# Kernel tuning notes

Measured on AMD Instinct MI355X. Metric: run time of the kernel, lower is better.

Reference implementation:

```python
import jax, jax.numpy as jnp
import numpy as np
import math

D_MODEL = 1024
N_HEADS = 16
D_HEAD = D_MODEL // N_HEADS  # 64
ROPE_BASE = 10000.0


def make_inv_freq(dim: int, base: float = ROPE_BASE) -> jnp.ndarray:
    half = dim // 2
    if half == 0:
        return jnp.zeros((1,), dtype=jnp.float32)
    return jnp.asarray(1.0 / base ** (np.arange(half, dtype=np.float32) * 2.0 / dim))


def rope_1d(x, pos, inv_freq):
    # x: (B, H, L, d_slice); pos: (B, 1, L)
    D = x.shape[-1]
    half = D // 2
    if half == 0:
        return x
    f = pos[..., None].astype(jnp.float32) * inv_freq  # (B,1,L,half)
    c, s = jnp.cos(f), jnp.sin(f)
    x1, x2 = x[..., :half], x[..., half:2 * half]
    out = jnp.concatenate([x1 * c - x2 * s, x2 * c + x1 * s], axis=-1)
    if D > 2 * half:
        out = jnp.concatenate([out, x[..., 2 * half:]], axis=-1)
    return out


def rope_3d(x, rows, cols, pairs):
    # x: (B, H, L, D_HEAD); rows/cols/pairs: (B, L)
    d_per = D_HEAD // 3
    d_row = D_HEAD - 2 * d_per  # 22
    d_col = d_per               # 21
    d1, d2 = d_row, d_row + d_col
    r = rows[:, None, :]
    c = cols[:, None, :]
    p = pairs[:, None, :]
    x_row = rope_1d(x[..., :d1], r, make_inv_freq(d_row))
    x_col = rope_1d(x[..., d1:d2], c, make_inv_freq(d_col))
    x_pair = rope_1d(x[..., d2:], p, make_inv_freq(d_per))
    return jnp.concatenate([x_row, x_col, x_pair], axis=-1)


def setup_inputs() -> dict:
    key = jax.random.key(0)
    ks = jax.random.split(key, 8)
    B, L, D = 2, 2048, D_MODEL
    x = jax.random.normal(ks[0], (B, L, D), dtype=jnp.float32)
    rows = jax.random.randint(ks[1], (B, L), 0, 30, dtype=jnp.int32)
    cols = jax.random.randint(ks[2], (B, L), 0, 30, dtype=jnp.int32)
    pairs = jax.random.randint(ks[3], (B, L), 0, 8, dtype=jnp.int32)
    key_padding_mask = jnp.ones((B, L), dtype=bool)
    scale = 0.02
    Wq = jax.random.normal(ks[4], (D, D), dtype=jnp.float32) * scale
    Wk = jax.random.normal(ks[5], (D, D), dtype=jnp.float32) * scale
    Wv = jax.random.normal(ks[6], (D, D), dtype=jnp.float32) * scale
    Wo = jax.random.normal(ks[7], (D, D), dtype=jnp.float32) * scale
    return {"x": x, "rows": rows, "cols": cols, "pairs": pairs,
            "key_padding_mask": key_padding_mask,
            "Wq": Wq, "Wk": Wk, "Wv": Wv, "Wo": Wo}


def reference(x, rows, cols, pairs, key_padding_mask, Wq, Wk, Wv, Wo):
    B, L, D = x.shape
    H, Dh = N_HEADS, D_HEAD
    # torch Linear (bias=False): y = x @ W.T, W: (out, in)
    q = jnp.einsum('bld,ed->ble', x, Wq).reshape(B, L, H, Dh).transpose(0, 2, 1, 3)
    k = jnp.einsum('bld,ed->ble', x, Wk).reshape(B, L, H, Dh).transpose(0, 2, 1, 3)
    v = jnp.einsum('bld,ed->ble', x, Wv).reshape(B, L, H, Dh).transpose(0, 2, 1, 3)
    # 3-axis RoPE per head (self-attention: same positions for q and k)
    q = rope_3d(q, rows, cols, pairs)
    k = rope_3d(k, rows, cols, pairs)
    scale = math.sqrt(Dh)
    scores = jnp.einsum('bhqd,bhkd->bhqk', q, k) / scale
    scores = jnp.where(key_padding_mask[:, None, None, :], scores, -jnp.inf)
    attn = jax.nn.softmax(scores, axis=-1)
    out = jnp.einsum('bhqk,bhkd->bhqd', attn, v)
    out = out.transpose(0, 2, 1, 3).reshape(B, L, D)
    return jnp.einsum('bld,ed->ble', out, Wo)
```

## Files before the change

kernel.cpp:

```cpp
#include <hip/hip_runtime.h>

typedef unsigned short ushort_t;
typedef __bf16 bf16x8 __attribute__((ext_vector_type(8)));
typedef float f32x4 __attribute__((ext_vector_type(4)));

#define LOG10K 9.210340371976184f
#define QSCALE 0.18033688011112042f

__device__ __forceinline__ unsigned short f2b(float f) {
  unsigned u = __float_as_uint(f);
  u += 0x7fffu + ((u >> 16) & 1u);
  return (unsigned short)(u >> 16);
}
__device__ __forceinline__ float b2f(unsigned short h) {
  return __uint_as_float(((unsigned)h) << 16);
}
__device__ __forceinline__ float exp2_fast(float x) {
  float r;
  asm("v_exp_f32 %0, %1" : "=v"(r) : "v"(x));
  return r;
}

__device__ __forceinline__ void async16(const void* g, void* l) {
  __builtin_amdgcn_global_load_lds(
      (const __attribute__((address_space(1))) unsigned int*)g,
      (__attribute__((address_space(3))) unsigned int*)l, 16, 0, 0);
}

__global__ void cvt_f32_bf16(const float* __restrict__ src, ushort_t* __restrict__ dst, int n4) {
  int i = blockIdx.x * blockDim.x + threadIdx.x;
  int stride = gridDim.x * blockDim.x;
  for (; i < n4; i += stride) {
    float4 v = ((const float4*)src)[i];
    ushort4 o;
    o.x = f2b(v.x); o.y = f2b(v.y); o.z = f2b(v.z); o.w = f2b(v.w);
    ((ushort4*)dst)[i] = o;
  }
}

__global__ void cvt_w4(const float* __restrict__ a, const float* __restrict__ b,
                       const float* __restrict__ c, const float* __restrict__ d,
                       ushort_t* __restrict__ dst) {
  int blk = blockIdx.x;
  int w = blk >> 10;
  int i = (blk & 1023) * 256 + threadIdx.x;
  const float* src = (w == 0) ? a : (w == 1) ? b : (w == 2) ? c : d;
  float4 v = ((const float4*)src)[i];
  ushort4 o;
  o.x = f2b(v.x); o.y = f2b(v.y); o.z = f2b(v.z); o.w = f2b(v.w);
  ((ushort4*)dst)[(size_t)w * 262144 + i] = o;
}

template<int OUTMODE>
__global__ __launch_bounds__(256) void gemm_bt(const ushort_t* __restrict__ A,
                                               const ushort_t* __restrict__ Bw,
                                               void* __restrict__ out,
                                               void* __restrict__ out2,
                                               void* __restrict__ out3,
                                               int M, int N, int K) {
  __shared__ ushort_t As[128 * 64];
  __shared__ ushort_t Bs[128 * 64];
  int tid = threadIdx.x;
  int w = tid >> 6, l = tid & 63, g = l >> 4, c = l & 15;
  int nbx = gridDim.x;
  int lin = blockIdx.y * nbx + blockIdx.x;
  int per = (nbx * gridDim.y) >> 3;
  int swz = (lin & 7) * per + (lin >> 3);
  int m0 = (swz / nbx) * 128, n0 = (swz % nbx) * 128;
  int wm = (w >> 1) * 64, wn = (w & 1) * 64;
  f32x4 acc[4][4] = {};

  for (int kt = 0; kt < K; kt += 64) {
#pragma unroll
    for (int cc = 0; cc < 4; ++cc) {
      int e = cc * 2048 + w * 512 + l * 8;
      int row = e >> 6;
      int jb = l & 7;
      int col = (jb ^ (row & 7)) << 3;
      async16(A + (size_t)(m0 + row) * K + kt + col, As + row * 64 + jb * 8);
      async16(Bw + (size_t)(n0 + row) * K + kt + col, Bs + row * 64 + jb * 8);
    }
    __syncthreads();
#pragma unroll
    for (int s = 0; s < 2; ++s) {
      bf16x8 af[4], bfr[4];
#pragma unroll
      for (int mi = 0; mi < 4; ++mi) {
        int row = wm + mi * 16 + c;
        int blk = (s * 4 + g) ^ (row & 7);
        af[mi] = *(const bf16x8*)(const void*)(As + row * 64 + blk * 8);
      }
#pragma unroll
      for (int ni = 0; ni < 4; ++ni) {
        int row = wn + ni * 16 + c;
        int blk = (s * 4 + g) ^ (row & 7);
        bfr[ni] = *(const bf16x8*)(const void*)(Bs + row * 64 + blk * 8);
      }
#pragma unroll
      for (int mi = 0; mi < 4; ++mi)
#pragma unroll
        for (int ni = 0; ni < 4; ++ni)
          acc[mi][ni] = __builtin_amdgcn_mfma_f32_16x16x32_bf16(af[mi], bfr[ni], acc[mi][ni], 0, 0, 0);
    }
    __syncthreads();
  }

#pragma unroll
  for (int mi = 0; mi < 4; ++mi) {
#pragma unroll
    for (int ni = 0; ni < 4; ++ni) {
      int mrow0 = m0 + wm + mi * 16 + g * 4;
      int ncol = n0 + wn + ni * 16 + c;
      if (OUTMODE == 3) {
        int sec = ncol >> 10;
        int nn = ncol & 1023;
        int h = nn >> 6, d = nn & 63;
        int b = mrow0 >> 11, ll0 = mrow0 & 2047;
        if (sec == 2) {
          ushort4 o;
          o.x = f2b(acc[mi][ni][0]); o.y = f2b(acc[mi][ni][1]);
          o.z = f2b(acc[mi][ni][2]); o.w = f2b(acc[mi][ni][3]);
          *(ushort4*)((ushort_t*)out3 + ((size_t)(b * 16 + h) * 64 + d) * 2048 + ll0) = o;
        } else {
          ushort_t* dst = (ushort_t*)(sec ? out2 : out);
#pragma unroll
          for (int j = 0; j < 4; ++j)
            dst[((size_t)(b * 16 + h) * 2048 + ll0 + j) * 64 + d] = f2b(acc[mi][ni][j]);
        }
      } else {
#pragma unroll
        for (int j = 0; j < 4; ++j)
          ((float*)out)[(size_t)(mrow0 + j) * N + ncol] = acc[mi][ni][j];
      }
    }
  }
}

__global__ void rope_qk(ushort_t* __restrict__ Qg, ushort_t* __restrict__ Kg,
                        const int* __restrict__ rows, const int* __restrict__ cols,
                        const int* __restrict__ pairs) {
  __shared__ float tl[1420];
  for (int i = threadIdx.x; i < 710; i += 256) {
    float ang;
    if (i < 330) {
      int p = i / 11, k = i - p * 11;
      ang = (float)p * __expf(-(LOG10K / 11.0f) * (float)k);
    } else if (i < 630) {
      int r = i - 330;
      int p = r / 10, k = r - p * 10;
      ang = (float)p * __expf(-(LOG10K * 2.0f / 21.0f) * (float)k);
    } else {
      int r = i - 630;
      int p = r / 10, k = r - p * 10;
      ang = (float)p * __expf(-(LOG10K * 2.0f / 21.0f) * (float)k);
    }
    float s, cs;
    sincosf(ang, &s, &cs);
    tl[2 * i] = cs;
    tl[2 * i + 1] = s;
  }
  __syncthreads();
  const float2* rt = (const float2*)tl;
  const float2* ct = (const float2*)(tl + 660);
  const float2* pt = (const float2*)(tl + 1260);

  int idx = blockIdx.x * blockDim.x + threadIdx.x;
  int which = idx >> 16;
  int r = idx & 65535;
  int b = r >> 15;
  int h = (r >> 11) & 15;
  int ll = r & 2047;
  ushort_t* base = (which ? Kg : Qg) + ((size_t)(b * 16 + h) * 2048 + ll) * 64;

  float f[64];
  const uint4* p = (const uint4*)base;
#pragma unroll
  for (int t = 0; t < 8; ++t) {
    uint4 v = p[t];
    unsigned a0 = v.x, a1 = v.y, a2 = v.z, a3 = v.w;
    f[t * 8 + 0] = b2f((unsigned short)(a0 & 0xffff)); f[t * 8 + 1] = b2f((unsigned short)(a0 >> 16));
    f[t * 8 + 2] = b2f((unsigned short)(a1 & 0xffff)); f[t * 8 + 3] = b2f((unsigned short)(a1 >> 16));
    f[t * 8 + 4] = b2f((unsigned short)(a2 & 0xffff)); f[t * 8 + 5] = b2f((unsigned short)(a2 >> 16));
    f[t * 8 + 6] = b2f((unsigned short)(a3 & 0xffff)); f[t * 8 + 7] = b2f((unsigned short)(a3 >> 16));
  }

  int bl = b * 2048 + ll;
  int pr = rows[bl], pc = cols[bl], pp = pairs[bl];

#pragma unroll
  for (int i = 0; i < 11; ++i) {
    float2 cs = rt[pr * 11 + i];
    float x1 = f[i], x2 = f[i + 11];
    f[i] = x1 * cs.x - x2 * cs.y;
    f[i + 11] = x2 * cs.x + x1 * cs.y;
  }
#pragma unroll
  for (int i = 0; i < 10; ++i) {
    float2 cs = ct[pc * 10 + i];
    float x1 = f[22 + i], x2 = f[32 + i];
    f[22 + i] = x1 * cs.x - x2 * cs.y;
    f[32 + i] = x2 * cs.x + x1 * cs.y;
    float2 cs2 = pt[pp * 10 + i];
    x1 = f[43 + i]; x2 = f[53 + i];
    f[43 + i] = x1 * cs2.x - x2 * cs2.y;
    f[53 + i] = x2 * cs2.x + x1 * cs2.y;
  }
  if (which == 0) {
#pragma unroll
    for (int i = 0; i < 64; ++i) f[i] *= QSCALE;
  }

  uint4* po = (uint4*)base;
#pragma unroll
  for (int t = 0; t < 8; ++t) {
    uint4 v;
    v.x = (unsigned)f2b(f[t * 8 + 0]) | ((unsigned)f2b(f[t * 8 + 1]) << 16);
    v.y = (unsigned)f2b(f[t * 8 + 2]) | ((unsigned)f2b(f[t * 8 + 3]) << 16);
    v.z = (unsigned)f2b(f[t * 8 + 4]) | ((unsigned)f2b(f[t * 8 + 5]) << 16);
    v.w = (unsigned)f2b(f[t * 8 + 6]) | ((unsigned)f2b(f[t * 8 + 7]) << 16);
    po[t] = v;
  }
}

__global__ __launch_bounds__(512) void flash_attn(const ushort_t* __restrict__ Qg,
                                                  const ushort_t* __restrict__ Kg,
                                                  const ushort_t* __restrict__ Vt,
                                                  ushort_t* __restrict__ AO) {
  __shared__ ushort_t Kl[2][4096];
  __shared__ ushort_t Vl[2][4096];
  __shared__ ushort_t Pl[8][1024];
  int bid = blockIdx.x;
  int wg = (bid & 7) * 64 + (bid >> 3);
  int bh = wg >> 4, qt = wg & 15;
  int tid = threadIdx.x;
  int w = tid >> 6, l = tid & 63, g = l >> 4, c = l & 15;

  const ushort_t* Qbase = Qg + ((size_t)bh * 2048 + qt * 128 + w * 16) * 64;
  bf16x8 qf[2];
#pragma unroll
  for (int s = 0; s < 2; ++s)
    qf[s] = *(const bf16x8*)(const void*)(Qbase + c * 64 + s * 32 + g * 8);

  f32x4 acc[4] = {};
  float mrow = -1e30f;
  float lrow = 0.f;

  char* KlB = (char*)&Kl[0][0];
  char* VlB = (char*)&Vl[0][0];
  char* PlW = (char*)&Pl[w][0];
  int c7 = c & 7;
  int c7_4 = c7 << 4;
  int offA0 = c * 128 + ((g ^ c7) << 4);
  int offA1 = c * 128 + (((4 ^ g) ^ c7) << 4);
  char* prow = PlW + c * 128;

  int srow = tid >> 3, sjb = tid & 7;
  int scol = (sjb ^ (srow & 7)) << 3;
  char* Kdst = KlB + srow * 128 + sjb * 16;
  char* Vdst = VlB + srow * 128 + sjb * 16;
  const ushort_t* Ksrc = Kg + ((size_t)bh * 2048 + srow) * 64 + scol;
  const ushort_t* Vsrc = Vt + ((size_t)bh * 64 + srow) * 2048 + scol;

  async16(Ksrc, Kdst);
  async16(Vsrc, Vdst);
  Ksrc += 4096; Vsrc += 64;
  asm volatile("s_waitcnt vmcnt(0)" ::: "memory");
  __syncthreads();

  int bufoff = 0;
  for (int kt = 0; kt < 32; ++kt) {
    if (kt < 31) {
      async16(Ksrc, Kdst + (bufoff ^ 8192));
      async16(Vsrc, Vdst + (bufoff ^ 8192));
      Ksrc += 4096; Vsrc += 64;
    }
    const char* KA0 = KlB + bufoff + offA0;
    const char* KA1 = KlB + bufoff + offA1;
    const char* VA0 = VlB + bufoff + offA0;
    const char* VA1 = VlB + bufoff + offA1;

    f32x4 sc[4] = {};
    __builtin_amdgcn_s_setprio(1);
#pragma unroll
    for (int kb = 0; kb < 4; ++kb) {
      bf16x8 a0 = *(const bf16x8*)(const void*)(KA0 + kb * 2048);
      bf16x8 a1 = *(const bf16x8*)(const void*)(KA1 + kb * 2048);
      sc[kb] = __builtin_amdgcn_mfma_f32_16x16x32_bf16(a0, qf[0], sc[kb], 0, 0, 0);
      sc[kb] = __builtin_amdgcn_mfma_f32_16x16x32_bf16(a1, qf[1], sc[kb], 0, 0, 0);
    }
    __builtin_amdgcn_s_setprio(0);

    {
      float t = sc[0][0];
#pragma unroll
      for (int kb = 0; kb < 4; ++kb)
#pragma unroll
        for (int j = 0; j < 4; ++j) t = fmaxf(t, sc[kb][j]);
      t = fmaxf(t, __shfl_xor(t, 16));
      t = fmaxf(t, __shfl_xor(t, 32));
      if (!__all(t - mrow <= 8.0f)) {
        float mnew = fmaxf(mrow, t);
        float corr = exp2_fast(mrow - mnew);
        mrow = mnew;
        lrow *= corr;
#pragma unroll
        for (int j = 0; j < 4; ++j) {
          float cj = __shfl(corr, ((l >> 4) << 2) | j);
#pragma unroll
          for (int db = 0; db < 4; ++db) acc[db][j] *= cj;
        }
      }
      float m = mrow;
      float ps = 0.f;
#pragma unroll
      for (int kb = 0; kb < 4; ++kb) {
        float p0 = exp2_fast(sc[kb][0] - m);
        float p1 = exp2_fast(sc[kb][1] - m);
        float p2 = exp2_fast(sc[kb][2] - m);
        float p3 = exp2_fast(sc[kb][3] - m);
        ps += (p0 + p1) + (p2 + p3);
        unsigned r0, r1;
        asm("v_cvt_pk_bf16_f32 %0, %1, %2" : "=v"(r0) : "v"(p0), "v"(p1));
        asm("v_cvt_pk_bf16_f32 %0, %1, %2" : "=v"(r1) : "v"(p2), "v"(p3));
        uint2 pr; pr.x = r0; pr.y = r1;
        *(uint2*)(prow + ((kb * 32 + g * 8) ^ c7_4)) = pr;
      }
      ps += __shfl_xor(ps, 16);
      ps += __shfl_xor(ps, 32);
      lrow += ps;
    }
    asm volatile("s_waitcnt lgkmcnt(0)" ::: "memory");

    __builtin_amdgcn_s_setprio(1);
#pragma unroll
    for (int s2 = 0; s2 < 2; ++s2) {
      bf16x8 pf = *(const bf16x8*)(const void*)(prow + ((s2 * 64 + g * 16) ^ c7_4));
      const char* VA = s2 ? VA1 : VA0;
#pragma unroll
      for (int db = 0; db < 4; ++db) {
        bf16x8 vf = *(const bf16x8*)(const void*)(VA + db * 2048);
        acc[db] = __builtin_amdgcn_mfma_f32_16x16x32_bf16(pf, vf, acc[db], 0, 0, 0);
      }
    }
    __builtin_amdgcn_s_setprio(0);

    asm volatile("s_waitcnt vmcnt(0)" ::: "memory");
    __syncthreads();
    bufoff ^= 8192;
  }

  int b = bh >> 4, h = bh & 15;
  {
    float linv = 1.0f / lrow;
#pragma unroll
    for (int j = 0; j < 4; ++j) {
      float inv = __shfl(linv, ((l >> 4) << 2) | j);
      int token = qt * 128 + w * 16 + g * 4 + j;
      size_t rowbase = (size_t)(b * 2048 + token) * 1024 + h * 64;
#pragma unroll
      for (int db = 0; db < 4; ++db)
        AO[rowbase + db * 16 + c] = f2b(acc[db][j] * inv);
    }
  }
}

extern "C" void kernel_launch(void* const* d_in, const int* in_sizes, int n_in,
                              void* d_out, int out_size, void* d_ws, size_t ws_size,
                              hipStream_t stream) {
  const float* x = (const float*)d_in[0];
  const int* rows = (const int*)d_in[1];
  const int* cols = (const int*)d_in[2];
  const int* pairs = (const int*)d_in[3];
  const float* Wq = (const float*)d_in[5];
  const float* Wk = (const float*)d_in[6];
  const float* Wv = (const float*)d_in[7];
  const float* Wo = (const float*)d_in[8];

  char* ws = (char*)d_ws;
  ushort_t* xb   = (ushort_t*)(ws);
  ushort_t* Wqkv = (ushort_t*)(ws + (8u << 20));
  ushort_t* Wob  = Wqkv + 3u * 1048576u;
  ushort_t* Qg   = (ushort_t*)(ws + (16u << 20));
  ushort_t* Kg   = (ushort_t*)(ws + (24u << 20));
  ushort_t* Vt   = (ushort_t*)(ws + (32u << 20));
  ushort_t* AO   = (ushort_t*)(ws);

  cvt_f32_bf16<<<1024, 256, 0, stream>>>(x, xb, 4194304 / 4);
  cvt_w4<<<4096, 256, 0, stream>>>(Wq, Wk, Wv, Wo, Wqkv);

  dim3 gg3(24, 32);
  gemm_bt<3><<<gg3, 256, 0, stream>>>(xb, Wqkv, Qg, Kg, Vt, 4096, 3072, 1024);

  rope_qk<<<512, 256, 0, stream>>>(Qg, Kg, rows, cols, pairs);

  flash_attn<<<512, 512, 0, stream>>>(Qg, Kg, Vt, AO);

  dim3 gg2(8, 32);
  gemm_bt<2><<<gg2, 256, 0, stream>>>(AO, Wob, d_out, nullptr, nullptr, 4096, 1024, 1024);
}
```

Before: 131.1 us.

## Triple-buffer K/V tiles, defer row-sum reduction, and fuse conversion kernels

New measurement: 125.4 us. 1.05x faster.

```diff
diff --git a/kernel.cpp b/kernel.cpp
--- a/kernel.cpp
+++ b/kernel.cpp
@@ -27,28 +27,29 @@
       (__attribute__((address_space(3))) unsigned int*)l, 16, 0, 0);
 }
 
-__global__ void cvt_f32_bf16(const float* __restrict__ src, ushort_t* __restrict__ dst, int n4) {
-  int i = blockIdx.x * blockDim.x + threadIdx.x;
-  int stride = gridDim.x * blockDim.x;
-  for (; i < n4; i += stride) {
-    float4 v = ((const float4*)src)[i];
+__global__ void cvt_all(const float* __restrict__ x, const float* __restrict__ a,
+                        const float* __restrict__ b, const float* __restrict__ cw,
+                        const float* __restrict__ d,
+                        ushort_t* __restrict__ xb, ushort_t* __restrict__ wb) {
+  int i = blockIdx.x * 256 + threadIdx.x;
+#pragma unroll
+  for (int it = 0; it < 2; ++it) {
+    int idx = i + it * 524288;
+    float4 v = ((const float4*)x)[idx];
     ushort4 o;
     o.x = f2b(v.x); o.y = f2b(v.y); o.z = f2b(v.z); o.w = f2b(v.w);
-    ((ushort4*)dst)[i] = o;
-  }
-}
-
-__global__ void cvt_w4(const float* __restrict__ a, const float* __restrict__ b,
-                       const float* __restrict__ c, const float* __restrict__ d,
-                       ushort_t* __restrict__ dst) {
-  int blk = blockIdx.x;
-  int w = blk >> 10;
-  int i = (blk & 1023) * 256 + threadIdx.x;
-  const float* src = (w == 0) ? a : (w == 1) ? b : (w == 2) ? c : d;
-  float4 v = ((const float4*)src)[i];
-  ushort4 o;
-  o.x = f2b(v.x); o.y = f2b(v.y); o.z = f2b(v.z); o.w = f2b(v.w);
-  ((ushort4*)dst)[(size_t)w * 262144 + i] = o;
+    ((ushort4*)xb)[idx] = o;
+  }
+#pragma unroll
+  for (int it = 0; it < 2; ++it) {
+    int idx = i + it * 524288;
+    int w = idx >> 18, off = idx & 262143;
+    const float* src = (w == 0) ? a : (w == 1) ? b : (w == 2) ? cw : d;
+    float4 v = ((const float4*)src)[off];
+    ushort4 o;
+    o.x = f2b(v.x); o.y = f2b(v.y); o.z = f2b(v.z); o.w = f2b(v.w);
+    ((ushort4*)wb)[idx] = o;
+  }
 }
 
 template<int OUTMODE>
@@ -226,8 +227,8 @@
                                                   const ushort_t* __restrict__ Kg,
                                                   const ushort_t* __restrict__ Vt,
                                                   ushort_t* __restrict__ AO) {
-  __shared__ ushort_t Kl[2][4096];
-  __shared__ ushort_t Vl[2][4096];
+  __shared__ ushort_t Kl[3][4096];
+  __shared__ ushort_t Vl[3][4096];
   __shared__ ushort_t Pl[8][1024];
   int bid = blockIdx.x;
   int wg = (bid & 7) * 64 + (bid >> 3);
@@ -243,7 +244,7 @@
 
   f32x4 acc[4] = {};
   float mrow = -1e30f;
-  float lrow = 0.f;
+  float lsum = 0.f;
 
   char* KlB = (char*)&Kl[0][0];
   char* VlB = (char*)&Vl[0][0];
@@ -261,23 +262,28 @@
   const ushort_t* Ksrc = Kg + ((size_t)bh * 2048 + srow) * 64 + scol;
   const ushort_t* Vsrc = Vt + ((size_t)bh * 64 + srow) * 2048 + scol;
 
-  async16(Ksrc, Kdst);
-  async16(Vsrc, Vdst);
-  Ksrc += 4096; Vsrc += 64;
-  asm volatile("s_waitcnt vmcnt(0)" ::: "memory");
+  auto STAGE = [&](int off) {
+    async16(Ksrc, Kdst + off);
+    async16(Vsrc, Vdst + off);
+    Ksrc += 4096; Vsrc += 64;
+  };
+
+  STAGE(0);
+  STAGE(8192);
+  asm volatile("s_waitcnt vmcnt(2)" ::: "memory");
   __syncthreads();
 
-  int bufoff = 0;
+  int cur = 0;
   for (int kt = 0; kt < 32; ++kt) {
-    if (kt < 31) {
-      async16(Ksrc, Kdst + (bufoff ^ 8192));
-      async16(Vsrc, Vdst + (bufoff ^ 8192));
-      Ksrc += 4096; Vsrc += 64;
-    }
-    const char* KA0 = KlB + bufoff + offA0;
-    const char* KA1 = KlB + bufoff + offA1;
-    const char* VA0 = VlB + bufoff + offA0;
-    const char* VA1 = VlB + bufoff + offA1;
+    if (kt < 30) {
+      int stg = cur + 16384;
+      if (stg >= 24576) stg -= 24576;
+      STAGE(stg);
+    }
+    const char* KA0 = KlB + cur + offA0;
+    const char* KA1 = KlB + cur + offA1;
+    const char* VA0 = VlB + cur + offA0;
+    const char* VA1 = VlB + cur + offA1;
 
     f32x4 sc[4] = {};
     __builtin_amdgcn_s_setprio(1);
@@ -296,13 +302,13 @@
       for (int kb = 0; kb < 4; ++kb)
 #pragma unroll
         for (int j = 0; j < 4; ++j) t = fmaxf(t, sc[kb][j]);
-      t = fmaxf(t, __shfl_xor(t, 16));
-      t = fmaxf(t, __shfl_xor(t, 32));
       if (!__all(t - mrow <= 8.0f)) {
+        t = fmaxf(t, __shfl_xor(t, 16));
+        t = fmaxf(t, __shfl_xor(t, 32));
         float mnew = fmaxf(mrow, t);
         float corr = exp2_fast(mrow - mnew);
         mrow = mnew;
-        lrow *= corr;
+        lsum *= corr;
 #pragma unroll
         for (int j = 0; j < 4; ++j) {
           float cj = __shfl(corr, ((l >> 4) << 2) | j);
@@ -325,9 +331,7 @@
         uint2 pr; pr.x = r0; pr.y = r1;
         *(uint2*)(prow + ((kb * 32 + g * 8) ^ c7_4)) = pr;
       }
-      ps += __shfl_xor(ps, 16);
-      ps += __shfl_xor(ps, 32);
-      lrow += ps;
+      lsum += ps;
     }
     asm volatile("s_waitcnt lgkmcnt(0)" ::: "memory");
 
@@ -344,14 +348,22 @@
     }
     __builtin_amdgcn_s_setprio(0);
 
-    asm volatile("s_waitcnt vmcnt(0)" ::: "memory");
+    if (kt < 30) {
+      asm volatile("s_waitcnt vmcnt(2)" ::: "memory");
+    } else {
+      asm volatile("s_waitcnt vmcnt(0)" ::: "memory");
+    }
     __syncthreads();
-    bufoff ^= 8192;
+    cur += 8192;
+    if (cur == 24576) cur = 0;
   }
 
   int b = bh >> 4, h = bh & 15;
   {
-    float linv = 1.0f / lrow;
+    float tot = lsum;
+    tot += __shfl_xor(tot, 16);
+    tot += __shfl_xor(tot, 32);
+    float linv = 1.0f / tot;
 #pragma unroll
     for (int j = 0; j < 4; ++j) {
       float inv = __shfl(linv, ((l >> 4) << 2) | j);
@@ -385,8 +397,7 @@
   ushort_t* Vt   = (ushort_t*)(ws + (32u << 20));
   ushort_t* AO   = (ushort_t*)(ws);
 
-  cvt_f32_bf16<<<1024, 256, 0, stream>>>(x, xb, 4194304 / 4);
-  cvt_w4<<<4096, 256, 0, stream>>>(Wq, Wk, Wv, Wo, Wqkv);
+  cvt_all<<<2048, 256, 0, stream>>>(x, Wq, Wk, Wv, Wo, xb, Wqkv);
 
   dim3 gg3(24, 32);
   gemm_bt<3><<<gg3, 256, 0, stream>>>(xb, Wqkv, Qg, Kg, Vt, 4096, 3072, 1024);
```
